# Kernel tuning notes

Hardware: AMD Instinct MI355X
Metric: run time of the kernel (lower is better)

## Reference

```python
import jax, jax.numpy as jnp
import numpy as np

B = 16384

def setup_inputs() -> dict:
    key = jax.random.key(0)
    ks = jax.random.split(key, 10)
    def lin(kw, fan_in, fan_out):
        lim = 1.0 / np.sqrt(fan_in)
        k1, k2 = jax.random.split(kw)
        w = jax.random.uniform(k1, (fan_out, fan_in), jnp.float32, -lim, lim)
        b = jax.random.uniform(k2, (fan_out,), jnp.float32, -lim, lim)
        return w, b
    x = jax.random.normal(ks[0], (B, 784), dtype=jnp.float32)
    conv_w = jnp.ones((3, 3), dtype=jnp.float32)
    w1, b1 = lin(ks[1], 676, 256)
    w2, b2 = lin(ks[2], 256, 128)
    w3, b3 = lin(ks[3], 128, 64)
    w4, b4 = lin(ks[4], 64, 10)
    return {"x": x, "conv_w": conv_w, "w1": w1, "b1": b1, "w2": w2, "b2": b2,
            "w3": w3, "b3": b3, "w4": w4, "b4": b4}

def reference(x, conv_w, w1, b1, w2, b2, w3, b3, w4, b4):
    b = x.shape[0]
    img = x.reshape(b, 1, 28, 28)                      # NCHW
    kern = conv_w.reshape(1, 1, 3, 3)                   # OIHW
    conv = jax.lax.conv_general_dilated(
        img, kern, window_strides=(1, 1), padding='VALID',
        dimension_numbers=('NCHW', 'OIHW', 'NCHW'))     # [B,1,26,26]
    h = conv.reshape(b, 26 * 26)
    h1 = jax.nn.relu(h @ w1.T + b1)
    h2 = jax.nn.relu(h1 @ w2.T + b2)
    h3 = jax.nn.relu(h2 @ w3.T + b3)
    out = h3 @ w4.T + b4                                # [B,10] logits
    return out
```

## Files before the change

kernel.cpp:

```cpp
#include <hip/hip_runtime.h>
#include <hip/hip_bf16.h>

typedef __attribute__((ext_vector_type(8))) short bf16x8;
typedef __attribute__((ext_vector_type(4))) float f32x4;

__device__ __forceinline__ unsigned short f2bf(float f) {
  unsigned int u = __builtin_bit_cast(unsigned int, f);
  u += 0x7fffu + ((u >> 16) & 1u);
  return (unsigned short)(u >> 16);
}

__device__ __forceinline__ f32x4 mfma16(bf16x8 a, bf16x8 b, f32x4 c) {
  return __builtin_amdgcn_mfma_f32_16x16x32_bf16(a, b, c, 0, 0, 0);
}

__global__ __launch_bounds__(256) void prep_weights(
    const float* __restrict__ w1, const float* __restrict__ w2,
    const float* __restrict__ w3, const float* __restrict__ w4,
    const float* __restrict__ cw,
    unsigned short* __restrict__ w1p, unsigned short* __restrict__ w2b,
    unsigned short* __restrict__ w3b, unsigned short* __restrict__ w4b) {
  __shared__ float wrow[676];
  __shared__ float cws[9];
  const int o = blockIdx.x;
  const int t = threadIdx.x;
  if (t < 9) cws[t] = cw[t];
  for (int i = t; i < 676; i += 256) wrow[i] = w1[o * 676 + i];
  __syncthreads();
#pragma unroll
  for (int it = 0; it < 4; ++it) {
    int p = t + it * 256;
    if (p < 800) {
      float acc = 0.f;
      if (p < 784) {
        int u = p / 28, v = p - u * 28;
#pragma unroll
        for (int a = 0; a < 3; ++a) {
          int ii = u - a;
          if (ii < 0 || ii >= 26) continue;
#pragma unroll
          for (int b = 0; b < 3; ++b) {
            int jj = v - b;
            if (jj < 0 || jj >= 26) continue;
            acc += cws[a * 3 + b] * wrow[26 * ii + jj];
          }
        }
      }
      w1p[o * 800 + p] = f2bf(acc);
    }
  }
  const int idx = o * 256 + t;
  const int stride = 256 * 256;
  for (int i = idx; i < 128 * 256; i += stride) w2b[i] = f2bf(w2[i]);
  for (int i = idx; i < 64 * 128; i += stride) w3b[i] = f2bf(w3[i]);
  for (int i = idx; i < 16 * 64; i += stride) {
    int oo = i >> 6, k = i & 63;
    w4b[i] = f2bf(oo < 10 ? w4[oo * 64 + k] : 0.f);
  }
}

__global__ __launch_bounds__(512, 4) void fused_mlp(
    const float* __restrict__ x,
    const unsigned short* __restrict__ w1p,
    const unsigned short* __restrict__ w2b,
    const unsigned short* __restrict__ w3b,
    const unsigned short* __restrict__ w4b,
    const float* __restrict__ b1, const float* __restrict__ b2,
    const float* __restrict__ b3, const float* __restrict__ b4,
    float* __restrict__ out)
{
  __shared__ unsigned short lds_s[25856];
  unsigned short* xs  = lds_s;
  unsigned short* h1s = lds_s;
  unsigned short* h2s = lds_s + 12800;
  unsigned short* h3s = lds_s + 20480;

  const int tid = threadIdx.x;
  const int lane = tid & 63;
  const int lane15 = lane & 15;
  const int kg = (lane >> 4) << 3;
  const int w = tid >> 6;
  const int row0 = blockIdx.x * 32;
  const int rb = (lane >> 4) << 2;

  const unsigned short* bp = w1p + (w * 32 + lane15) * 800 + kg;
  bf16x8 b0a = *(const bf16x8*)(bp);
  bf16x8 b0b = *(const bf16x8*)(bp + 16 * 800);
  bf16x8 b1a = *(const bf16x8*)(bp + 32);
  bf16x8 b1b = *(const bf16x8*)(bp + 16 * 800 + 32);
  bf16x8 b2a = *(const bf16x8*)(bp + 64);
  bf16x8 b2b = *(const bf16x8*)(bp + 16 * 800 + 64);

  {
    const float* xblk = x + (size_t)row0 * 784;
    for (int f = tid; f < 32 * 196; f += 512) {
      int rr = f / 196, c4 = f - rr * 196;
      float4 v = *(const float4*)(xblk + rr * 784 + (c4 << 2));
      unsigned int p0 = (unsigned)f2bf(v.x) | ((unsigned)f2bf(v.y) << 16);
      unsigned int p1 = (unsigned)f2bf(v.z) | ((unsigned)f2bf(v.w) << 16);
      unsigned int* dst = (unsigned int*)(xs + rr * 808 + (c4 << 2));
      dst[0] = p0;
      dst[1] = p1;
    }
    if (tid < 256) {
      int rr = tid >> 3, u = tid & 7;
      *(unsigned int*)(xs + rr * 808 + 784 + (u << 1)) = 0u;
    }
  }
  __syncthreads();

  f32x4 acc1[2][2] = {};
  {
    const unsigned short* a0p = xs + lane15 * 808 + kg;
    const unsigned short* a1p = xs + (16 + lane15) * 808 + kg;
#pragma unroll
    for (int ks = 0; ks < 25; ++ks) {
      bf16x8 u0 = b0a, u1 = b0b;
      b0a = b1a; b0b = b1b;
      b1a = b2a; b1b = b2b;
      if (ks + 3 < 25) {
        b2a = *(const bf16x8*)(bp + (ks + 3) * 32);
        b2b = *(const bf16x8*)(bp + 16 * 800 + (ks + 3) * 32);
      }
      bf16x8 a0 = *(const bf16x8*)(a0p + ks * 32);
      bf16x8 a1 = *(const bf16x8*)(a1p + ks * 32);
      acc1[0][0] = mfma16(a0, u0, acc1[0][0]);
      acc1[1][0] = mfma16(a1, u0, acc1[1][0]);
      acc1[0][1] = mfma16(a0, u1, acc1[0][1]);
      acc1[1][1] = mfma16(a1, u1, acc1[1][1]);
    }
  }
  __syncthreads();

#pragma unroll
  for (int n = 0; n < 2; ++n) {
    const int col = w * 32 + n * 16 + lane15;
    const float bias = b1[col];
#pragma unroll
    for (int m = 0; m < 2; ++m) {
#pragma unroll
      for (int r = 0; r < 4; ++r) {
        float v = acc1[m][n][r] + bias;
        v = v > 0.f ? v : 0.f;
        h1s[(rb + m * 16 + r) * 264 + col] = f2bf(v);
      }
    }
  }
  __syncthreads();

  f32x4 acc2[2] = {};
  {
    const unsigned short* a0p = h1s + lane15 * 264 + kg;
    const unsigned short* a1p = h1s + (16 + lane15) * 264 + kg;
    const unsigned short* bp2 = w2b + (w * 16 + lane15) * 256 + kg;
#pragma unroll
    for (int ks = 0; ks < 8; ++ks) {
      const int k0 = ks << 5;
      bf16x8 a0 = *(const bf16x8*)(a0p + k0);
      bf16x8 a1 = *(const bf16x8*)(a1p + k0);
      bf16x8 fb = *(const bf16x8*)(bp2 + k0);
      acc2[0] = mfma16(a0, fb, acc2[0]);
      acc2[1] = mfma16(a1, fb, acc2[1]);
    }
  }
  {
    const int col = w * 16 + lane15;
    const float bias = b2[col];
#pragma unroll
    for (int m = 0; m < 2; ++m) {
#pragma unroll
      for (int r = 0; r < 4; ++r) {
        float v = acc2[m][r] + bias;
        v = v > 0.f ? v : 0.f;
        h2s[(rb + m * 16 + r) * 136 + col] = f2bf(v);
      }
    }
  }
  __syncthreads();

  f32x4 acc3 = {};
  {
    const int mh = w >> 2, cq = w & 3;
    const unsigned short* ap = h2s + (mh * 16 + lane15) * 136 + kg;
    const unsigned short* bp3 = w3b + (cq * 16 + lane15) * 128 + kg;
#pragma unroll
    for (int ks = 0; ks < 4; ++ks) {
      const int k0 = ks << 5;
      bf16x8 a0 = *(const bf16x8*)(ap + k0);
      bf16x8 fb = *(const bf16x8*)(bp3 + k0);
      acc3 = mfma16(a0, fb, acc3);
    }
    const int col = cq * 16 + lane15;
    const float bias = b3[col];
#pragma unroll
    for (int r = 0; r < 4; ++r) {
      float v = acc3[r] + bias;
      v = v > 0.f ? v : 0.f;
      h3s[(mh * 16 + rb + r) * 72 + col] = f2bf(v);
    }
  }
  __syncthreads();

  if (w < 2) {
    f32x4 acc4 = {};
    const unsigned short* ap = h3s + (w * 16 + lane15) * 72 + kg;
    const unsigned short* bp4 = w4b + lane15 * 64 + kg;
#pragma unroll
    for (int ks = 0; ks < 2; ++ks) {
      const int k0 = ks << 5;
      bf16x8 a0 = *(const bf16x8*)(ap + k0);
      bf16x8 fb = *(const bf16x8*)(bp4 + k0);
      acc4 = mfma16(a0, fb, acc4);
    }
    const int col = lane15;
    if (col < 10) {
      const float bias = b4[col];
#pragma unroll
      for (int r = 0; r < 4; ++r) {
        out[(size_t)(row0 + w * 16 + rb + r) * 10 + col] = acc4[r] + bias;
      }
    }
  }
}

extern "C" void kernel_launch(void* const* d_in, const int* in_sizes, int n_in,
                              void* d_out, int out_size, void* d_ws, size_t ws_size,
                              hipStream_t stream) {
  const float* x  = (const float*)d_in[0];
  const float* cw = (const float*)d_in[1];
  const float* w1 = (const float*)d_in[2];
  const float* b1 = (const float*)d_in[3];
  const float* w2 = (const float*)d_in[4];
  const float* b2 = (const float*)d_in[5];
  const float* w3 = (const float*)d_in[6];
  const float* b3 = (const float*)d_in[7];
  const float* w4 = (const float*)d_in[8];
  const float* b4 = (const float*)d_in[9];
  float* out = (float*)d_out;

  unsigned short* w1p = (unsigned short*)d_ws;
  unsigned short* w2b = w1p + 256 * 800;
  unsigned short* w3b = w2b + 128 * 256;
  unsigned short* w4b = w3b + 64 * 128;

  hipLaunchKernelGGL(prep_weights, dim3(256), dim3(256), 0, stream,
                     w1, w2, w3, w4, cw, w1p, w2b, w3b, w4b);

  hipLaunchKernelGGL(fused_mlp, dim3(512), dim3(512), 0, stream,
                     x, w1p, w2b, w3b, w4b, b1, b2, b3, b4, out);
}
```

Baseline: 121.9 us.

## Shrink row tile to 16 rows per block with 4 waves over wider columns

Each block now handles 16 batch rows with 256 threads (4 waves), and each wave covers 64 output columns of layer 1 instead of 32. The grid doubles to 1024 blocks and LDS per block halves, which gives better CU coverage and occupancy on a GPU with many CUs. In exchange, each w1 weight fragment is reused across only 16 rows, so global/L2 weight traffic per output row roughly doubles. Weight prefetch depth drops from three stages to two.

```diff
diff --git a/kernel.cpp b/kernel.cpp
--- a/kernel.cpp
+++ b/kernel.cpp
@@ -59,7 +59,7 @@
   }
 }
 
-__global__ __launch_bounds__(512, 4) void fused_mlp(
+__global__ __launch_bounds__(256, 6) void fused_mlp(
     const float* __restrict__ x,
     const unsigned short* __restrict__ w1p,
     const unsigned short* __restrict__ w2b,
@@ -69,31 +69,33 @@
     const float* __restrict__ b3, const float* __restrict__ b4,
     float* __restrict__ out)
 {
-  __shared__ unsigned short lds_s[25856];
+  __shared__ unsigned short lds_s[12928];
   unsigned short* xs  = lds_s;
   unsigned short* h1s = lds_s;
-  unsigned short* h2s = lds_s + 12800;
-  unsigned short* h3s = lds_s + 20480;
+  unsigned short* h2s = lds_s + 4352;
+  unsigned short* h3s = lds_s + 6656;
 
   const int tid = threadIdx.x;
   const int lane = tid & 63;
   const int lane15 = lane & 15;
   const int kg = (lane >> 4) << 3;
   const int w = tid >> 6;
-  const int row0 = blockIdx.x * 32;
+  const int row0 = blockIdx.x * 16;
   const int rb = (lane >> 4) << 2;
 
-  const unsigned short* bp = w1p + (w * 32 + lane15) * 800 + kg;
-  bf16x8 b0a = *(const bf16x8*)(bp);
-  bf16x8 b0b = *(const bf16x8*)(bp + 16 * 800);
-  bf16x8 b1a = *(const bf16x8*)(bp + 32);
-  bf16x8 b1b = *(const bf16x8*)(bp + 16 * 800 + 32);
-  bf16x8 b2a = *(const bf16x8*)(bp + 64);
-  bf16x8 b2b = *(const bf16x8*)(bp + 16 * 800 + 64);
+  const unsigned short* bp = w1p + (w * 64 + lane15) * 800 + kg;
+  bf16x8 bA0 = *(const bf16x8*)(bp);
+  bf16x8 bA1 = *(const bf16x8*)(bp + 16 * 800);
+  bf16x8 bA2 = *(const bf16x8*)(bp + 32 * 800);
+  bf16x8 bA3 = *(const bf16x8*)(bp + 48 * 800);
+  bf16x8 bB0 = *(const bf16x8*)(bp + 32);
+  bf16x8 bB1 = *(const bf16x8*)(bp + 16 * 800 + 32);
+  bf16x8 bB2 = *(const bf16x8*)(bp + 32 * 800 + 32);
+  bf16x8 bB3 = *(const bf16x8*)(bp + 48 * 800 + 32);
 
   {
     const float* xblk = x + (size_t)row0 * 784;
-    for (int f = tid; f < 32 * 196; f += 512) {
+    for (int f = tid; f < 16 * 196; f += 256) {
       int rr = f / 196, c4 = f - rr * 196;
       float4 v = *(const float4*)(xblk + rr * 784 + (c4 << 2));
       unsigned int p0 = (unsigned)f2bf(v.x) | ((unsigned)f2bf(v.y) << 16);
@@ -102,48 +104,45 @@
       dst[0] = p0;
       dst[1] = p1;
     }
-    if (tid < 256) {
+    if (tid < 128) {
       int rr = tid >> 3, u = tid & 7;
       *(unsigned int*)(xs + rr * 808 + 784 + (u << 1)) = 0u;
     }
   }
   __syncthreads();
 
-  f32x4 acc1[2][2] = {};
+  f32x4 acc1[4] = {};
   {
     const unsigned short* a0p = xs + lane15 * 808 + kg;
-    const unsigned short* a1p = xs + (16 + lane15) * 808 + kg;
 #pragma unroll
     for (int ks = 0; ks < 25; ++ks) {
-      bf16x8 u0 = b0a, u1 = b0b;
-      b0a = b1a; b0b = b1b;
-      b1a = b2a; b1b = b2b;
-      if (ks + 3 < 25) {
-        b2a = *(const bf16x8*)(bp + (ks + 3) * 32);
-        b2b = *(const bf16x8*)(bp + 16 * 800 + (ks + 3) * 32);
+      bf16x8 u0 = bA0, u1 = bA1, u2 = bA2, u3 = bA3;
+      bA0 = bB0; bA1 = bB1; bA2 = bB2; bA3 = bB3;
+      if (ks + 2 < 25) {
+        const unsigned short* p = bp + (ks + 2) * 32;
+        bB0 = *(const bf16x8*)(p);
+        bB1 = *(const bf16x8*)(p + 16 * 800);
+        bB2 = *(const bf16x8*)(p + 32 * 800);
+        bB3 = *(const bf16x8*)(p + 48 * 800);
       }
       bf16x8 a0 = *(const bf16x8*)(a0p + ks * 32);
-      bf16x8 a1 = *(const bf16x8*)(a1p + ks * 32);
-      acc1[0][0] = mfma16(a0, u0, acc1[0][0]);
-      acc1[1][0] = mfma16(a1, u0, acc1[1][0]);
-      acc1[0][1] = mfma16(a0, u1, acc1[0][1]);
-      acc1[1][1] = mfma16(a1, u1, acc1[1][1]);
-    }
-  }
-  __syncthreads();
-
-#pragma unroll
-  for (int n = 0; n < 2; ++n) {
-    const int col = w * 32 + n * 16 + lane15;
+      acc1[0] = mfma16(a0, u0, acc1[0]);
+      acc1[1] = mfma16(a0, u1, acc1[1]);
+      acc1[2] = mfma16(a0, u2, acc1[2]);
+      acc1[3] = mfma16(a0, u3, acc1[3]);
+    }
+  }
+  __syncthreads();
+
+#pragma unroll
+  for (int n = 0; n < 4; ++n) {
+    const int col = w * 64 + n * 16 + lane15;
     const float bias = b1[col];
 #pragma unroll
-    for (int m = 0; m < 2; ++m) {
-#pragma unroll
-      for (int r = 0; r < 4; ++r) {
-        float v = acc1[m][n][r] + bias;
-        v = v > 0.f ? v : 0.f;
-        h1s[(rb + m * 16 + r) * 264 + col] = f2bf(v);
-      }
+    for (int r = 0; r < 4; ++r) {
+      float v = acc1[n][r] + bias;
+      v = v > 0.f ? v : 0.f;
+      h1s[(rb + r) * 264 + col] = f2bf(v);
     }
   }
   __syncthreads();
@@ -151,73 +150,69 @@
   f32x4 acc2[2] = {};
   {
     const unsigned short* a0p = h1s + lane15 * 264 + kg;
-    const unsigned short* a1p = h1s + (16 + lane15) * 264 + kg;
-    const unsigned short* bp2 = w2b + (w * 16 + lane15) * 256 + kg;
+    const unsigned short* bp2 = w2b + (w * 32 + lane15) * 256 + kg;
 #pragma unroll
     for (int ks = 0; ks < 8; ++ks) {
       const int k0 = ks << 5;
       bf16x8 a0 = *(const bf16x8*)(a0p + k0);
-      bf16x8 a1 = *(const bf16x8*)(a1p + k0);
-      bf16x8 fb = *(const bf16x8*)(bp2 + k0);
-      acc2[0] = mfma16(a0, fb, acc2[0]);
-      acc2[1] = mfma16(a1, fb, acc2[1]);
-    }
-  }
-  {
-    const int col = w * 16 + lane15;
+      bf16x8 f0 = *(const bf16x8*)(bp2 + k0);
+      bf16x8 f1 = *(const bf16x8*)(bp2 + 16 * 256 + k0);
+      acc2[0] = mfma16(a0, f0, acc2[0]);
+      acc2[1] = mfma16(a0, f1, acc2[1]);
+    }
+  }
+#pragma unroll
+  for (int n = 0; n < 2; ++n) {
+    const int col = w * 32 + n * 16 + lane15;
     const float bias = b2[col];
 #pragma unroll
-    for (int m = 0; m < 2; ++m) {
-#pragma unroll
-      for (int r = 0; r < 4; ++r) {
-        float v = acc2[m][r] + bias;
-        v = v > 0.f ? v : 0.f;
-        h2s[(rb + m * 16 + r) * 136 + col] = f2bf(v);
-      }
+    for (int r = 0; r < 4; ++r) {
+      float v = acc2[n][r] + bias;
+      v = v > 0.f ? v : 0.f;
+      h2s[(rb + r) * 136 + col] = f2bf(v);
     }
   }
   __syncthreads();
 
   f32x4 acc3 = {};
   {
-    const int mh = w >> 2, cq = w & 3;
-    const unsigned short* ap = h2s + (mh * 16 + lane15) * 136 + kg;
-    const unsigned short* bp3 = w3b + (cq * 16 + lane15) * 128 + kg;
+    const unsigned short* a0p = h2s + lane15 * 136 + kg;
+    const unsigned short* bp3 = w3b + (w * 16 + lane15) * 128 + kg;
 #pragma unroll
     for (int ks = 0; ks < 4; ++ks) {
       const int k0 = ks << 5;
-      bf16x8 a0 = *(const bf16x8*)(ap + k0);
-      bf16x8 fb = *(const bf16x8*)(bp3 + k0);
-      acc3 = mfma16(a0, fb, acc3);
-    }
-    const int col = cq * 16 + lane15;
+      bf16x8 a0 = *(const bf16x8*)(a0p + k0);
+      bf16x8 f0 = *(const bf16x8*)(bp3 + k0);
+      acc3 = mfma16(a0, f0, acc3);
+    }
+    const int col = w * 16 + lane15;
     const float bias = b3[col];
 #pragma unroll
     for (int r = 0; r < 4; ++r) {
       float v = acc3[r] + bias;
       v = v > 0.f ? v : 0.f;
-      h3s[(mh * 16 + rb + r) * 72 + col] = f2bf(v);
-    }
-  }
-  __syncthreads();
-
-  if (w < 2) {
+      h3s[(rb + r) * 72 + col] = f2bf(v);
+    }
+  }
+  __syncthreads();
+
+  if (w == 0) {
     f32x4 acc4 = {};
-    const unsigned short* ap = h3s + (w * 16 + lane15) * 72 + kg;
+    const unsigned short* ap = h3s + lane15 * 72 + kg;
     const unsigned short* bp4 = w4b + lane15 * 64 + kg;
 #pragma unroll
     for (int ks = 0; ks < 2; ++ks) {
       const int k0 = ks << 5;
       bf16x8 a0 = *(const bf16x8*)(ap + k0);
-      bf16x8 fb = *(const bf16x8*)(bp4 + k0);
-      acc4 = mfma16(a0, fb, acc4);
+      bf16x8 f0 = *(const bf16x8*)(bp4 + k0);
+      acc4 = mfma16(a0, f0, acc4);
     }
     const int col = lane15;
     if (col < 10) {
       const float bias = b4[col];
 #pragma unroll
       for (int r = 0; r < 4; ++r) {
-        out[(size_t)(row0 + w * 16 + rb + r) * 10 + col] = acc4[r] + bias;
+        out[(size_t)(row0 + rb + r) * 10 + col] = acc4[r] + bias;
       }
     }
   }
@@ -246,6 +241,6 @@
   hipLaunchKernelGGL(prep_weights, dim3(256), dim3(256), 0, stream,
                      w1, w2, w3, w4, cw, w1p, w2b, w3b, w4b);
 
-  hipLaunchKernelGGL(fused_mlp, dim3(512), dim3(512), 0, stream,
+  hipLaunchKernelGGL(fused_mlp, dim3(1024), dim3(256), 0, stream,
                      x, w1p, w2b, w3b, w4b, b1, b2, b3, b4, out);
 }
```

Result: slower. 139.4 us (+14.4%).
